# Performance work log

Measured on AMD Instinct MI355X. Metric: run time of the kernel, lower is better.

## Reference

```python
import jax, jax.numpy as jnp
import numpy as np

B = 8192; N = 50; NUM_NODES = 200000; NUM_EDGES = 1000000
FEAT = 64; EFEAT = 4; TD = 16; D = 64


def setup_inputs() -> dict:
    key = jax.random.key(0)
    ks = jax.random.split(key, 32)
    p = lambda i, shape: jax.random.normal(ks[i], shape, jnp.float32) * 0.05
    inp = {}
    nf = jax.random.normal(ks[0], (NUM_NODES, FEAT), jnp.float32)
    skills = jax.random.randint(ks[1], (NUM_NODES,), 0, 100).astype(jnp.float32)
    inp['node_raw_features'] = nf.at[:, 0].set(skills)  # col 0 = skill id
    inp['edge_raw_features'] = jax.random.normal(ks[2], (NUM_EDGES, EFEAT), jnp.float32)
    inp['src_node_ids'] = jax.random.randint(ks[3], (B,), 0, NUM_NODES)
    inp['dst_node_ids'] = jax.random.randint(ks[4], (B,), 0, NUM_NODES)
    inp['node_interact_times'] = jax.random.uniform(ks[5], (B,), jnp.float32, 0.0, 1e4)
    inp['src_neighbor_node_ids'] = jax.random.randint(ks[6], (B, N), 0, NUM_NODES)
    inp['src_neighbor_edge_ids'] = jax.random.randint(ks[7], (B, N), 0, NUM_EDGES)
    inp['src_neighbor_times'] = jax.random.uniform(ks[8], (B, N), jnp.float32, 0.0, 1e4)
    inp['dst_neighbor_node_ids'] = jax.random.randint(ks[9], (B, N), 0, NUM_NODES)
    inp['dst_neighbor_edge_ids'] = jax.random.randint(ks[10], (B, N), 0, NUM_EDGES)
    inp['dst_neighbor_times'] = jax.random.uniform(ks[11], (B, N), jnp.float32, 0.0, 1e4)
    # projection layers
    inp['W_feat'] = p(12, (FEAT, D)); inp['b_feat'] = p(13, (D,))
    inp['W_edge'] = p(14, (1, D));    inp['b_edge'] = p(15, (D,))
    inp['W_time'] = p(16, (TD, D));   inp['b_time'] = p(17, (D,))
    inp['W_struct'] = p(18, (1, D));  inp['b_struct'] = p(19, (D,))
    inp['W_out'] = p(20, (D, D));     inp['b_out'] = p(21, (D,))
    # time encoder (cos(w*dt + b), trainable Linear(1, TD) as in TGN TimeEncoder)
    inp['time_w'] = p(22, (TD,)); inp['time_b'] = p(23, (TD,))
    # src / dst GRUs (PyTorch layout: W_ih [3H,E], W_hh [3H,H])
    inp['src_W_ih'] = p(24, (3 * D, D)); inp['src_W_hh'] = p(25, (3 * D, D))
    inp['src_b_ih'] = p(26, (3 * D,));   inp['src_b_hh'] = p(27, (3 * D,))
    inp['dst_W_ih'] = p(28, (3 * D, D)); inp['dst_W_hh'] = p(29, (3 * D, D))
    inp['dst_b_ih'] = p(30, (3 * D,));   inp['dst_b_hh'] = p(31, (3 * D,))
    return inp


def _lin(x, W, b):
    return x @ W + b


def _gru_last_hidden(x, W_ih, W_hh, b_ih, b_hh):
    # x: [B, T, E] -> final hidden state [B, H] (PyTorch GRU equations)
    Bb, _, _ = x.shape
    H = W_hh.shape[1]

    def step(h, xt):
        gi = xt @ W_ih.T + b_ih            # [B, 3H]
        gh = h @ W_hh.T + b_hh             # [B, 3H]
        ir, iz, inn = jnp.split(gi, 3, axis=-1)
        hr, hz, hn = jnp.split(gh, 3, axis=-1)
        r = jax.nn.sigmoid(ir + hr)
        z = jax.nn.sigmoid(iz + hz)
        n = jnp.tanh(inn + r * hn)
        h_new = (1.0 - z) * n + z * h
        return h_new, None

    h0 = jnp.zeros((Bb, H), x.dtype)
    hT, _ = jax.lax.scan(step, h0, jnp.swapaxes(x, 0, 1))
    return hT


def reference(node_raw_features, edge_raw_features, src_node_ids, dst_node_ids,
              node_interact_times, src_neighbor_node_ids, src_neighbor_edge_ids,
              src_neighbor_times, dst_neighbor_node_ids, dst_neighbor_edge_ids,
              dst_neighbor_times, W_feat, b_feat, W_edge, b_edge, W_time, b_time,
              W_struct, b_struct, W_out, b_out, time_w, time_b,
              src_W_ih, src_W_hh, src_b_ih, src_b_hh,
              dst_W_ih, dst_W_hh, dst_b_ih, dst_b_hh):
    t = node_interact_times
    # append the query interaction itself (edge id 0) -> [B, N+1]
    src_nids = jnp.concatenate([src_neighbor_node_ids, src_node_ids[:, None]], 1)
    src_eids = jnp.concatenate([src_neighbor_edge_ids, jnp.zeros_like(src_node_ids)[:, None]], 1)
    src_ts = jnp.concatenate([src_neighbor_times, t[:, None]], 1)
    dst_nids = jnp.concatenate([dst_neighbor_node_ids, dst_node_ids[:, None]], 1)
    dst_eids = jnp.concatenate([dst_neighbor_edge_ids, jnp.zeros_like(dst_node_ids)[:, None]], 1)
    dst_ts = jnp.concatenate([dst_neighbor_times, t[:, None]], 1)

    # co-occurrence features [B, N, 1]
    co_src = (src_neighbor_node_ids == dst_node_ids[:, None]).astype(jnp.float32)[..., None]
    co_dst = (dst_neighbor_node_ids == src_node_ids[:, None]).astype(jnp.float32)[..., None]
    # skill match features [B, N, 1]
    src_skill = node_raw_features[src_nids][:, :-1, 0].astype(jnp.int32)
    dst_skill = node_raw_features[dst_nids][:, -1, 0].astype(jnp.int32)[:, None]
    skill_f = (src_skill == dst_skill).astype(jnp.float32)[..., None]

    src_struct = _lin(co_src, W_struct, b_struct)
    dst_struct = _lin(co_dst, W_struct, b_struct)
    skill_struct = _lin(skill_f, W_struct, b_struct)

    def get_feats(nids, eids, ts):
        node_f = _lin(node_raw_features[nids], W_feat, b_feat)        # [B,N+1,D]
        delta = t[:, None] - ts                                       # dual-decay ablation: delta times
        tenc = jnp.cos(delta[..., None] * time_w + time_b)            # [B,N+1,TD]
        time_f = _lin(tenc, W_time, b_time)                           # [B,N+1,D]
        edge_f = _lin(edge_raw_features[eids][..., :1], W_edge, b_edge)
        return node_f, edge_f, time_f

    sn, se, st = get_feats(src_nids, src_eids, src_ts)
    dn, de, dt = get_feats(dst_nids, dst_eids, dst_ts)
    src_feats = sn + se + st
    dst_feats = dn + de + dt

    src_emb = _gru_last_hidden(src_feats[:, :-1] + skill_struct + src_struct,
                               src_W_ih, src_W_hh, src_b_ih, src_b_hh) + (se + st)[:, -1]
    dst_emb = _gru_last_hidden((de + dt)[:, :-1] + dst_struct,
                               dst_W_ih, dst_W_hh, dst_b_ih, dst_b_hh) + dst_feats[:, -1]

    return _lin(src_emb, W_out, b_out), _lin(dst_emb, W_out, b_out)
```

## Files before the change

### kernel.cpp

```cpp
#include <hip/hip_runtime.h>
#include <stdint.h>

#define BB 8192
#define NN 50

typedef _Float16 half8 __attribute__((ext_vector_type(8)));
typedef float floatx4 __attribute__((ext_vector_type(4)));

union FragU { uint4 u; half8 h; };
static __device__ __forceinline__ half8 u2h(uint4 u) { FragU f; f.u = u; return f.h; }

static __device__ __forceinline__ uint32_t pk2u(float a, float b) {
    auto p = __builtin_amdgcn_cvt_pkrtz(a, b);
    uint32_t u; __builtin_memcpy(&u, &p, 4); return u;
}

#define MFMA(A, B, C) __builtin_amdgcn_mfma_f32_16x16x32_f16((A), (B), (C), 0, 0, 0)

static __device__ __forceinline__ float fsig(float x)   { return 1.0f / (1.0f + __expf(-x)); }
static __device__ __forceinline__ float ftanhf(float x) { return 1.0f - 2.0f / (__expf(2.0f * x) + 1.0f); }

__global__ __launch_bounds__(256, 1)
void dygkt3(const float* __restrict__ nodef, const float* __restrict__ edgef,
            const int* __restrict__ src_ids, const int* __restrict__ dst_ids,
            const float* __restrict__ times,
            const int* __restrict__ s_nids, const int* __restrict__ s_eids,
            const float* __restrict__ s_ts,
            const int* __restrict__ d_nids, const int* __restrict__ d_eids,
            const float* __restrict__ d_ts,
            const float* __restrict__ W_feat, const float* __restrict__ b_feat,
            const float* __restrict__ W_edge, const float* __restrict__ b_edge,
            const float* __restrict__ W_time, const float* __restrict__ b_time,
            const float* __restrict__ W_str,  const float* __restrict__ b_str,
            const float* __restrict__ W_out,  const float* __restrict__ b_out,
            const float* __restrict__ time_w, const float* __restrict__ time_b,
            const float* __restrict__ sWih, const float* __restrict__ sWhh,
            const float* __restrict__ sbih, const float* __restrict__ sbhh,
            const float* __restrict__ dWih, const float* __restrict__ dWhh,
            const float* __restrict__ dbih, const float* __restrict__ dbhh,
            float* __restrict__ out)
{
    __shared__ uint4 wfA[8][64];
    __shared__ uint4 woA[8][64];
    __shared__ __align__(16) _Float16 xbuf[4][16 * 72];
    __shared__ __align__(16) _Float16 hbuf[4][16 * 72];

    const int tid = threadIdx.x, wave = tid >> 6, lane = tid & 63;
    const int g = lane >> 4, i16 = lane & 15;
    const bool is_src = blockIdx.x < 128;
    const int ib0 = (int)(blockIdx.x & 127) * 64 + wave * 16;
    const int b = ib0 + i16;

    for (int q = tid; q < 512; q += 256) {
        int l = q & 63, tt = q >> 6;
        int kh = tt >> 2, mt = tt & 3, gg = l >> 4, ii = l & 15;
        float v[8], w[8];
        #pragma unroll
        for (int j = 0; j < 8; ++j) {
            int k = 32 * kh + 8 * gg + j, m = 16 * mt + ii;
            v[j] = W_feat[k * 64 + m];
            w[j] = W_out[k * 64 + m];
        }
        wfA[tt][l] = make_uint4(pk2u(v[0],v[1]), pk2u(v[2],v[3]), pk2u(v[4],v[5]), pk2u(v[6],v[7]));
        woA[tt][l] = make_uint4(pk2u(w[0],w[1]), pk2u(w[2],w[3]), pk2u(w[4],w[5]), pk2u(w[6],w[7]));
    }
    for (int q = tid; q < 4 * 16 * 72 / 2; q += 256) ((uint32_t*)hbuf)[q] = 0;
    __syncthreads();

    const float* WI = is_src ? sWih : dWih;
    const float* WH = is_src ? sWhh : dWhh;
    uint4 wih[12][2], whh[12][2];
    #pragma unroll
    for (int mt = 0; mt < 12; ++mt)
        #pragma unroll
        for (int kh = 0; kh < 2; ++kh) {
            const float* p = WI + (size_t)(16 * mt + i16) * 64 + 32 * kh + 8 * g;
            float4 a = *(const float4*)p, c = *(const float4*)(p + 4);
            wih[mt][kh] = make_uint4(pk2u(a.x,a.y), pk2u(a.z,a.w), pk2u(c.x,c.y), pk2u(c.z,c.w));
            const float* q = WH + (size_t)(16 * mt + i16) * 64 + 32 * kh + 8 * g;
            float4 e = *(const float4*)q, f = *(const float4*)(q + 4);
            whh[mt][kh] = make_uint4(pk2u(e.x,e.y), pk2u(e.z,e.w), pk2u(f.x,f.y), pk2u(f.z,f.w));
        }

    uint4 wtA[4];
    #pragma unroll
    for (int mt = 0; mt < 4; ++mt) {
        float v[8];
        #pragma unroll
        for (int j = 0; j < 8; ++j) {
            int k = 8 * g + j, dim = 16 * mt + i16;
            float x = 0.0f;
            if (k < 16)       x = W_time[k * 64 + dim];
            else if (k == 16) x = W_edge[dim];
            else if (k == 17) x = W_str[dim];
            else if (k == 18) x = b_edge[dim] + b_time[dim];
            else if (k == 19) x = is_src ? (b_feat[dim] + 2.0f * b_str[dim]) : b_str[dim];
            else if (k == 20) x = b_feat[dim];
            v[j] = x;
        }
        wtA[mt] = make_uint4(pk2u(v[0],v[1]), pk2u(v[2],v[3]), pk2u(v[4],v[5]), pk2u(v[6],v[7]));
    }

    const float* BI = is_src ? sbih : dbih;
    const float* BH = is_src ? sbhh : dbhh;
    floatx4 brz[8], bin[4], bhn[4];
    #pragma unroll
    for (int mt = 0; mt < 8; ++mt) {
        floatx4 v;
        #pragma unroll
        for (int r = 0; r < 4; ++r) v[r] = BI[16 * mt + 4 * g + r] + BH[16 * mt + 4 * g + r];
        brz[mt] = v;
    }
    #pragma unroll
    for (int mt = 0; mt < 4; ++mt) {
        floatx4 vi, vh;
        #pragma unroll
        for (int r = 0; r < 4; ++r) {
            vi[r] = BI[128 + 16 * mt + 4 * g + r];
            vh[r] = BH[128 + 16 * mt + 4 * g + r];
        }
        bin[mt] = vi; bhn[mt] = vh;
    }

    const int* pn = (is_src ? s_nids : d_nids) + (size_t)b * NN;
    const int* pe = (is_src ? s_eids : d_eids) + (size_t)b * NN;
    const float* pt = (is_src ? s_ts : d_ts) + (size_t)b * NN;
    const float tqL = times[b];
    const int didL = dst_ids[b];
    const int oid = is_src ? didL : src_ids[b];
    const float dskill = is_src ? nodef[(size_t)didL * 64] : 0.0f;
    float twc[8], tbc[8];
    #pragma unroll
    for (int j = 0; j < 8; ++j) {
        int k = 8 * (g & 1) + j;
        twc[j] = time_w[k]; tbc[j] = time_b[k];
    }

    int nidC = pn[0], eidC = pe[0];
    float tsC = pt[0];
    float e0C = edgef[4 * (size_t)eidC];
    float4 nfa = {0,0,0,0}, nfb = {0,0,0,0}, nfc = {0,0,0,0}, nfd = {0,0,0,0};
    if (is_src) {
        const float* rp = nodef + (size_t)nidC * 64 + 8 * g;
        nfa = *(const float4*)rp;        nfb = *(const float4*)(rp + 4);
        nfc = *(const float4*)(rp + 32); nfd = *(const float4*)(rp + 36);
    }

    floatx4 hM[4] = {{0,0,0,0},{0,0,0,0},{0,0,0,0},{0,0,0,0}};
    const floatx4 z4 = {0,0,0,0};
    _Float16* xb = xbuf[wave];
    _Float16* hb = hbuf[wave];

    for (int t = 0; t < NN; ++t) {
        int nidN = 0, eidN = 0; float tsN = 0.0f;
        if (t + 1 < NN) { nidN = pn[t + 1]; eidN = pe[t + 1]; tsN = pt[t + 1]; }

        float nsk = __shfl(nfa.x, i16);
        float sf = ((nidC == oid) ? 1.0f : 0.0f) +
                   ((is_src && nsk == dskill) ? 1.0f : 0.0f);
        float delta = tqL - tsC;
        uint4 tb4;
        if (g < 2) {
            float cv[8];
            #pragma unroll
            for (int j = 0; j < 8; ++j) cv[j] = __cosf(delta * twc[j] + tbc[j]);
            tb4 = make_uint4(pk2u(cv[0],cv[1]), pk2u(cv[2],cv[3]), pk2u(cv[4],cv[5]), pk2u(cv[6],cv[7]));
        } else if (g == 2) {
            tb4 = make_uint4(pk2u(e0C, sf), pk2u(1.0f, 1.0f), 0u, 0u);
        } else {
            tb4 = make_uint4(0u, 0u, 0u, 0u);
        }
        half8 tB = u2h(tb4);

        floatx4 xacc[4];
        if (is_src) {
            uint4 nf0 = make_uint4(pk2u(nfa.x,nfa.y), pk2u(nfa.z,nfa.w), pk2u(nfb.x,nfb.y), pk2u(nfb.z,nfb.w));
            uint4 nf1 = make_uint4(pk2u(nfc.x,nfc.y), pk2u(nfc.z,nfc.w), pk2u(nfd.x,nfd.y), pk2u(nfd.z,nfd.w));
            half8 nB0 = u2h(nf0), nB1 = u2h(nf1);
            #pragma unroll
            for (int mt = 0; mt < 4; ++mt) {
                floatx4 a = MFMA(u2h(wfA[mt][lane]), nB0, z4);
                a = MFMA(u2h(wfA[4 + mt][lane]), nB1, a);
                xacc[mt] = MFMA(u2h(wtA[mt]), tB, a);
            }
        } else {
            #pragma unroll
            for (int mt = 0; mt < 4; ++mt) xacc[mt] = MFMA(u2h(wtA[mt]), tB, z4);
        }

        #pragma unroll
        for (int mt = 0; mt < 4; ++mt)
            *(uint2*)&xb[i16 * 72 + mt * 16 + 4 * g] =
                make_uint2(pk2u(xacc[mt][0], xacc[mt][1]), pk2u(xacc[mt][2], xacc[mt][3]));
        half8 xB0 = u2h(*(const uint4*)&xb[i16 * 72 + 8 * g]);
        half8 xB1 = u2h(*(const uint4*)&xb[i16 * 72 + 32 + 8 * g]);

        float e0N = 0.0f; float4 na = {0,0,0,0}, nb = {0,0,0,0}, nc = {0,0,0,0}, nd = {0,0,0,0};
        if (t + 1 < NN) {
            e0N = edgef[4 * (size_t)eidN];
            if (is_src) {
                const float* rp = nodef + (size_t)nidN * 64 + 8 * g;
                na = *(const float4*)rp;        nb = *(const float4*)(rp + 4);
                nc = *(const float4*)(rp + 32); nd = *(const float4*)(rp + 36);
            }
        }

        half8 hB0 = u2h(*(const uint4*)&hb[i16 * 72 + 8 * g]);
        half8 hB1 = u2h(*(const uint4*)&hb[i16 * 72 + 32 + 8 * g]);

        floatx4 rg[4], zg[4], ia[4], ha[4];
        #pragma unroll
        for (int mt = 0; mt < 4; ++mt) {
            floatx4 a = MFMA(u2h(wih[mt][0]), xB0, brz[mt]);
            a = MFMA(u2h(wih[mt][1]), xB1, a);
            a = MFMA(u2h(whh[mt][0]), hB0, a);
            rg[mt] = MFMA(u2h(whh[mt][1]), hB1, a);
        }
        #pragma unroll
        for (int mt = 0; mt < 4; ++mt) {
            floatx4 a = MFMA(u2h(wih[4 + mt][0]), xB0, brz[4 + mt]);
            a = MFMA(u2h(wih[4 + mt][1]), xB1, a);
            a = MFMA(u2h(whh[4 + mt][0]), hB0, a);
            zg[mt] = MFMA(u2h(whh[4 + mt][1]), hB1, a);
        }
        #pragma unroll
        for (int mt = 0; mt < 4; ++mt) {
            floatx4 a = MFMA(u2h(wih[8 + mt][0]), xB0, bin[mt]);
            ia[mt] = MFMA(u2h(wih[8 + mt][1]), xB1, a);
            floatx4 c = MFMA(u2h(whh[8 + mt][0]), hB0, bhn[mt]);
            ha[mt] = MFMA(u2h(whh[8 + mt][1]), hB1, c);
        }

        #pragma unroll
        for (int mt = 0; mt < 4; ++mt)
            #pragma unroll
            for (int r = 0; r < 4; ++r) {
                float rr = fsig(rg[mt][r]);
                float zz = fsig(zg[mt][r]);
                float nn = ftanhf(ia[mt][r] + rr * ha[mt][r]);
                hM[mt][r] = nn + zz * (hM[mt][r] - nn);
            }

        #pragma unroll
        for (int mt = 0; mt < 4; ++mt)
            *(uint2*)&hb[i16 * 72 + mt * 16 + 4 * g] =
                make_uint2(pk2u(hM[mt][0], hM[mt][1]), pk2u(hM[mt][2], hM[mt][3]));

        nidC = nidN; eidC = eidN; tsC = tsN; e0C = e0N;
        nfa = na; nfb = nb; nfc = nc; nfd = nd;
    }

    float e00 = edgef[0];
    uint4 tt4;
    if (g < 2) {
        float cv[8];
        #pragma unroll
        for (int j = 0; j < 8; ++j) cv[j] = __cosf(tbc[j]);
        tt4 = make_uint4(pk2u(cv[0],cv[1]), pk2u(cv[2],cv[3]), pk2u(cv[4],cv[5]), pk2u(cv[6],cv[7]));
    } else if (g == 2) {
        tt4 = make_uint4(pk2u(e00, 0.0f), pk2u(1.0f, 0.0f), pk2u(is_src ? 0.0f : 1.0f, 0.0f), 0u);
    } else {
        tt4 = make_uint4(0u, 0u, 0u, 0u);
    }
    half8 tT = u2h(tt4);

    floatx4 tacc[4];
    #pragma unroll
    for (int mt = 0; mt < 4; ++mt) tacc[mt] = MFMA(u2h(wtA[mt]), tT, z4);
    if (!is_src) {
        const float* rp = nodef + (size_t)didL * 64 + 8 * g;
        float4 da = *(const float4*)rp,        db = *(const float4*)(rp + 4);
        float4 dc = *(const float4*)(rp + 32), dd = *(const float4*)(rp + 36);
        uint4 d0 = make_uint4(pk2u(da.x,da.y), pk2u(da.z,da.w), pk2u(db.x,db.y), pk2u(db.z,db.w));
        uint4 d1 = make_uint4(pk2u(dc.x,dc.y), pk2u(dc.z,dc.w), pk2u(dd.x,dd.y), pk2u(dd.z,dd.w));
        #pragma unroll
        for (int mt = 0; mt < 4; ++mt) {
            tacc[mt] = MFMA(u2h(wfA[mt][lane]), u2h(d0), tacc[mt]);
            tacc[mt] = MFMA(u2h(wfA[4 + mt][lane]), u2h(d1), tacc[mt]);
        }
    }

    #pragma unroll
    for (int mt = 0; mt < 4; ++mt) {
        floatx4 e = hM[mt] + tacc[mt];
        *(uint2*)&xb[i16 * 72 + mt * 16 + 4 * g] =
            make_uint2(pk2u(e[0], e[1]), pk2u(e[2], e[3]));
    }
    half8 eB0 = u2h(*(const uint4*)&xb[i16 * 72 + 8 * g]);
    half8 eB1 = u2h(*(const uint4*)&xb[i16 * 72 + 32 + 8 * g]);

    const size_t obase = (is_src ? 0 : (size_t)BB * 64) + (size_t)(ib0 + i16) * 64;
    #pragma unroll
    for (int mt = 0; mt < 4; ++mt) {
        floatx4 bo;
        #pragma unroll
        for (int r = 0; r < 4; ++r) bo[r] = b_out[16 * mt + 4 * g + r];
        floatx4 o = MFMA(u2h(woA[mt][lane]), eB0, bo);
        o = MFMA(u2h(woA[4 + mt][lane]), eB1, o);
        #pragma unroll
        for (int r = 0; r < 4; ++r)
            out[obase + 16 * mt + 4 * g + r] = o[r];
    }
}

extern "C" void kernel_launch(void* const* d_in, const int* in_sizes, int n_in,
                              void* d_out, int out_size, void* d_ws, size_t ws_size,
                              hipStream_t stream) {
    (void)in_sizes; (void)n_in; (void)d_ws; (void)ws_size; (void)out_size;
    const float* nodef  = (const float*)d_in[0];
    const float* edgef  = (const float*)d_in[1];
    const int*   srcid  = (const int*)  d_in[2];
    const int*   dstid  = (const int*)  d_in[3];
    const float* times  = (const float*)d_in[4];
    const int*   s_nids = (const int*)  d_in[5];
    const int*   s_eids = (const int*)  d_in[6];
    const float* s_ts   = (const float*)d_in[7];
    const int*   d_nids = (const int*)  d_in[8];
    const int*   d_eids = (const int*)  d_in[9];
    const float* d_ts   = (const float*)d_in[10];
    const float* W_feat = (const float*)d_in[11];
    const float* b_feat = (const float*)d_in[12];
    const float* W_edge = (const float*)d_in[13];
    const float* b_edge = (const float*)d_in[14];
    const float* W_time = (const float*)d_in[15];
    const float* b_time = (const float*)d_in[16];
    const float* W_str  = (const float*)d_in[17];
    const float* b_str  = (const float*)d_in[18];
    const float* W_out  = (const float*)d_in[19];
    const float* b_out  = (const float*)d_in[20];
    const float* time_w = (const float*)d_in[21];
    const float* time_b = (const float*)d_in[22];
    const float* sWih   = (const float*)d_in[23];
    const float* sWhh   = (const float*)d_in[24];
    const float* sbih   = (const float*)d_in[25];
    const float* sbhh   = (const float*)d_in[26];
    const float* dWih   = (const float*)d_in[27];
    const float* dWhh   = (const float*)d_in[28];
    const float* dbih   = (const float*)d_in[29];
    const float* dbhh   = (const float*)d_in[30];

    dim3 grid(256), block(256);
    dygkt3<<<grid, block, 0, stream>>>(
        nodef, edgef, srcid, dstid, times,
        s_nids, s_eids, s_ts, d_nids, d_eids, d_ts,
        W_feat, b_feat, W_edge, b_edge, W_time, b_time,
        W_str, b_str, W_out, b_out, time_w, time_b,
        sWih, sWhh, sbih, sbhh, dWih, dWhh, dbih, dbhh,
        (float*)d_out);
}
```

Baseline: 297.4 us.

## Fold input projections into GRU input weights and process two timesteps per iteration

Precomputes per block the products of the GRU input weights with W_feat and with the time/edge/struct/bias projections, stored in shared memory. Gate input preactivations then come directly from raw node features and time encodings, with no intermediate x vector. The loop handles two timesteps per iteration, computing both steps' input-gate contributions first and prefetching two steps ahead, which shortens the serial recurrent chain. The cost is fp16 rounding of the fused weights and gate inputs, a setup phase of MFMAs, and more registers and shared memory.

```diff
diff --git a/kernel.cpp b/kernel.cpp
--- a/kernel.cpp
+++ b/kernel.cpp
@@ -5,23 +5,34 @@
 #define NN 50
 
 typedef _Float16 half8 __attribute__((ext_vector_type(8)));
+typedef _Float16 half4v __attribute__((ext_vector_type(4)));
 typedef float floatx4 __attribute__((ext_vector_type(4)));
 
 union FragU { uint4 u; half8 h; };
 static __device__ __forceinline__ half8 u2h(uint4 u) { FragU f; f.u = u; return f.h; }
-
+union F2U { uint2 u; half4v h; };
+static __device__ __forceinline__ floatx4 up4(uint2 u) {
+    F2U f; f.u = u; floatx4 r;
+    r[0] = (float)f.h[0]; r[1] = (float)f.h[1]; r[2] = (float)f.h[2]; r[3] = (float)f.h[3];
+    return r;
+}
 static __device__ __forceinline__ uint32_t pk2u(float a, float b) {
     auto p = __builtin_amdgcn_cvt_pkrtz(a, b);
     uint32_t u; __builtin_memcpy(&u, &p, 4); return u;
 }
-
+static __device__ __forceinline__ uint2 pkx4(floatx4 v) {
+    return make_uint2(pk2u(v[0], v[1]), pk2u(v[2], v[3]));
+}
+static __device__ __forceinline__ uint4 pkf8(const float* p) {
+    float4 a = *(const float4*)p, b = *(const float4*)(p + 4);
+    return make_uint4(pk2u(a.x, a.y), pk2u(a.z, a.w), pk2u(b.x, b.y), pk2u(b.z, b.w));
+}
 #define MFMA(A, B, C) __builtin_amdgcn_mfma_f32_16x16x32_f16((A), (B), (C), 0, 0, 0)
-
 static __device__ __forceinline__ float fsig(float x)   { return 1.0f / (1.0f + __expf(-x)); }
 static __device__ __forceinline__ float ftanhf(float x) { return 1.0f - 2.0f / (__expf(2.0f * x) + 1.0f); }
 
 __global__ __launch_bounds__(256, 1)
-void dygkt3(const float* __restrict__ nodef, const float* __restrict__ edgef,
+void dygkt4(const float* __restrict__ nodef, const float* __restrict__ edgef,
             const int* __restrict__ src_ids, const int* __restrict__ dst_ids,
             const float* __restrict__ times,
             const int* __restrict__ s_nids, const int* __restrict__ s_eids,
@@ -40,88 +51,154 @@
             const float* __restrict__ dbih, const float* __restrict__ dbhh,
             float* __restrict__ out)
 {
-    __shared__ uint4 wfA[8][64];
-    __shared__ uint4 woA[8][64];
-    __shared__ __align__(16) _Float16 xbuf[4][16 * 72];
-    __shared__ __align__(16) _Float16 hbuf[4][16 * 72];
+    __shared__ _Float16 Gsh[192 * 72];
+    __shared__ _Float16 Bsh[192 * 40];
+    __shared__ uint4    woA[8][64];
+    __shared__ uint4    wtT[4][64];
+    __shared__ _Float16 hbuf[4 * 16 * 72];
 
     const int tid = threadIdx.x, wave = tid >> 6, lane = tid & 63;
     const int g = lane >> 4, i16 = lane & 15;
     const bool is_src = blockIdx.x < 128;
     const int ib0 = (int)(blockIdx.x & 127) * 64 + wave * 16;
     const int b = ib0 + i16;
+    const floatx4 z4 = {0, 0, 0, 0};
+
+    const float* WI = is_src ? sWih : dWih;
+    const float* WH = is_src ? sWhh : dWhh;
+    const float* BI = is_src ? sbih : dbih;
+    const float* BH = is_src ? sbhh : dbhh;
 
     for (int q = tid; q < 512; q += 256) {
         int l = q & 63, tt = q >> 6;
         int kh = tt >> 2, mt = tt & 3, gg = l >> 4, ii = l & 15;
-        float v[8], w[8];
+        float w[8];
+        #pragma unroll
+        for (int j = 0; j < 8; ++j)
+            w[j] = W_out[(32 * kh + 8 * gg + j) * 64 + 16 * mt + ii];
+        woA[tt][l] = make_uint4(pk2u(w[0],w[1]), pk2u(w[2],w[3]), pk2u(w[4],w[5]), pk2u(w[6],w[7]));
+    }
+    {
+        int l = tid & 63, mt = tid >> 6, gg = l >> 4, ii = l & 15;
+        float v[8];
         #pragma unroll
         for (int j = 0; j < 8; ++j) {
-            int k = 32 * kh + 8 * gg + j, m = 16 * mt + ii;
-            v[j] = W_feat[k * 64 + m];
-            w[j] = W_out[k * 64 + m];
-        }
-        wfA[tt][l] = make_uint4(pk2u(v[0],v[1]), pk2u(v[2],v[3]), pk2u(v[4],v[5]), pk2u(v[6],v[7]));
-        woA[tt][l] = make_uint4(pk2u(w[0],w[1]), pk2u(w[2],w[3]), pk2u(w[4],w[5]), pk2u(w[6],w[7]));
-    }
-    for (int q = tid; q < 4 * 16 * 72 / 2; q += 256) ((uint32_t*)hbuf)[q] = 0;
-    __syncthreads();
-
-    const float* WI = is_src ? sWih : dWih;
-    const float* WH = is_src ? sWhh : dWhh;
-    uint4 wih[12][2], whh[12][2];
-    #pragma unroll
-    for (int mt = 0; mt < 12; ++mt)
-        #pragma unroll
-        for (int kh = 0; kh < 2; ++kh) {
-            const float* p = WI + (size_t)(16 * mt + i16) * 64 + 32 * kh + 8 * g;
-            float4 a = *(const float4*)p, c = *(const float4*)(p + 4);
-            wih[mt][kh] = make_uint4(pk2u(a.x,a.y), pk2u(a.z,a.w), pk2u(c.x,c.y), pk2u(c.z,c.w));
-            const float* q = WH + (size_t)(16 * mt + i16) * 64 + 32 * kh + 8 * g;
-            float4 e = *(const float4*)q, f = *(const float4*)(q + 4);
-            whh[mt][kh] = make_uint4(pk2u(e.x,e.y), pk2u(e.z,e.w), pk2u(f.x,f.y), pk2u(f.z,f.w));
-        }
-
-    uint4 wtA[4];
-    #pragma unroll
-    for (int mt = 0; mt < 4; ++mt) {
-        float v[8];
-        #pragma unroll
-        for (int j = 0; j < 8; ++j) {
-            int k = 8 * g + j, dim = 16 * mt + i16;
+            int k = 8 * gg + j, dim = 16 * mt + ii;
             float x = 0.0f;
             if (k < 16)       x = W_time[k * 64 + dim];
             else if (k == 16) x = W_edge[dim];
             else if (k == 17) x = W_str[dim];
             else if (k == 18) x = b_edge[dim] + b_time[dim];
-            else if (k == 19) x = is_src ? (b_feat[dim] + 2.0f * b_str[dim]) : b_str[dim];
             else if (k == 20) x = b_feat[dim];
             v[j] = x;
         }
-        wtA[mt] = make_uint4(pk2u(v[0],v[1]), pk2u(v[2],v[3]), pk2u(v[4],v[5]), pk2u(v[6],v[7]));
-    }
-
-    const float* BI = is_src ? sbih : dbih;
-    const float* BH = is_src ? sbhh : dbhh;
-    floatx4 brz[8], bin[4], bhn[4];
-    #pragma unroll
-    for (int mt = 0; mt < 8; ++mt) {
+        wtT[mt][l] = make_uint4(pk2u(v[0],v[1]), pk2u(v[2],v[3]), pk2u(v[4],v[5]), pk2u(v[6],v[7]));
+    }
+    for (int q = tid; q < 2304; q += 256) ((uint32_t*)hbuf)[q] = 0;
+
+    uint4 whh[12][2];
+    #pragma unroll
+    for (int mt = 0; mt < 12; ++mt)
+        #pragma unroll
+        for (int kh = 0; kh < 2; ++kh)
+            whh[mt][kh] = pkf8(WH + (size_t)(16 * mt + i16) * 64 + 32 * kh + 8 * g);
+
+    if (is_src) {
+        for (int mt = wave; mt < 12; mt += 4) {
+            uint4 A0 = pkf8(WI + (size_t)(16 * mt + i16) * 64 + 8 * g);
+            uint4 A1 = pkf8(WI + (size_t)(16 * mt + i16) * 64 + 32 + 8 * g);
+            #pragma unroll
+            for (int nt = 0; nt < 4; ++nt) {
+                uint4 B0 = pkf8(W_feat + (size_t)(16 * nt + i16) * 64 + 8 * g);
+                uint4 B1 = pkf8(W_feat + (size_t)(16 * nt + i16) * 64 + 32 + 8 * g);
+                floatx4 D = MFMA(u2h(A1), u2h(B1), MFMA(u2h(A0), u2h(B0), z4));
+                #pragma unroll
+                for (int r = 0; r < 4; ++r)
+                    Gsh[(16 * mt + 4 * g + r) * 72 + 16 * nt + i16] = (_Float16)D[r];
+            }
+            #pragma unroll
+            for (int nt = 0; nt < 2; ++nt) {
+                uint4 bB[2];
+                #pragma unroll
+                for (int kh = 0; kh < 2; ++kh) {
+                    float v[8];
+                    #pragma unroll
+                    for (int jj = 0; jj < 8; ++jj) {
+                        int d = 32 * kh + 8 * g + jj;
+                        float x = 0.0f;
+                        if (nt == 0) x = W_time[i16 * 64 + d];
+                        else if (i16 == 0) x = W_edge[d];
+                        else if (i16 == 1) x = W_str[d];
+                        else if (i16 == 2) x = b_edge[d] + b_time[d] + b_feat[d] + 2.0f * b_str[d];
+                        v[jj] = x;
+                    }
+                    bB[kh] = make_uint4(pk2u(v[0],v[1]), pk2u(v[2],v[3]), pk2u(v[4],v[5]), pk2u(v[6],v[7]));
+                }
+                floatx4 D = MFMA(u2h(A1), u2h(bB[1]), MFMA(u2h(A0), u2h(bB[0]), z4));
+                if (nt == 1 && i16 == 2) {
+                    #pragma unroll
+                    for (int r = 0; r < 4; ++r)
+                        D[r] += BI[16 * mt + 4 * g + r] + (mt < 8 ? BH[16 * mt + 4 * g + r] : 0.0f);
+                }
+                #pragma unroll
+                for (int r = 0; r < 4; ++r)
+                    Bsh[(16 * mt + 4 * g + r) * 40 + 16 * nt + i16] = (_Float16)D[r];
+            }
+        }
+    } else {
+        for (int p = tid; p < 4096; p += 256) {
+            int m = p & 63, j = p >> 6;
+            Gsh[m * 72 + j] = (_Float16)W_feat[j * 64 + m];
+        }
+        for (int mt = wave; mt < 12; mt += 4) {
+            uint4 A0 = pkf8(WI + (size_t)(16 * mt + i16) * 64 + 8 * g);
+            uint4 A1 = pkf8(WI + (size_t)(16 * mt + i16) * 64 + 32 + 8 * g);
+            #pragma unroll
+            for (int nt = 0; nt < 2; ++nt) {
+                uint4 bB[2];
+                #pragma unroll
+                for (int kh = 0; kh < 2; ++kh) {
+                    float v[8];
+                    #pragma unroll
+                    for (int jj = 0; jj < 8; ++jj) {
+                        int d = 32 * kh + 8 * g + jj;
+                        float x = 0.0f;
+                        if (nt == 0) x = W_time[i16 * 64 + d];
+                        else if (i16 == 0) x = W_edge[d];
+                        else if (i16 == 1) x = W_str[d];
+                        else if (i16 == 2) x = b_edge[d] + b_time[d] + b_str[d];
+                        v[jj] = x;
+                    }
+                    bB[kh] = make_uint4(pk2u(v[0],v[1]), pk2u(v[2],v[3]), pk2u(v[4],v[5]), pk2u(v[6],v[7]));
+                }
+                floatx4 D = MFMA(u2h(A1), u2h(bB[1]), MFMA(u2h(A0), u2h(bB[0]), z4));
+                if (nt == 1 && i16 == 2) {
+                    #pragma unroll
+                    for (int r = 0; r < 4; ++r)
+                        D[r] += BI[16 * mt + 4 * g + r] + (mt < 8 ? BH[16 * mt + 4 * g + r] : 0.0f);
+                }
+                #pragma unroll
+                for (int r = 0; r < 4; ++r)
+                    Bsh[(16 * mt + 4 * g + r) * 40 + 16 * nt + i16] = (_Float16)D[r];
+            }
+        }
+    }
+    __syncthreads();
+
+    floatx4 bhn[4];
+    #pragma unroll
+    for (int mt = 0; mt < 4; ++mt) {
         floatx4 v;
         #pragma unroll
-        for (int r = 0; r < 4; ++r) v[r] = BI[16 * mt + 4 * g + r] + BH[16 * mt + 4 * g + r];
-        brz[mt] = v;
-    }
-    #pragma unroll
-    for (int mt = 0; mt < 4; ++mt) {
-        floatx4 vi, vh;
-        #pragma unroll
-        for (int r = 0; r < 4; ++r) {
-            vi[r] = BI[128 + 16 * mt + 4 * g + r];
-            vh[r] = BH[128 + 16 * mt + 4 * g + r];
-        }
-        bin[mt] = vi; bhn[mt] = vh;
-    }
-
+        for (int r = 0; r < 4; ++r) v[r] = BH[128 + 16 * mt + 4 * g + r];
+        bhn[mt] = v;
+    }
+    float twc[8], tbc[8];
+    #pragma unroll
+    for (int j = 0; j < 8; ++j) {
+        twc[j] = time_w[8 * (g & 1) + j];
+        tbc[j] = time_b[8 * (g & 1) + j];
+    }
     const int* pn = (is_src ? s_nids : d_nids) + (size_t)b * NN;
     const int* pe = (is_src ? s_eids : d_eids) + (size_t)b * NN;
     const float* pt = (is_src ? s_ts : d_ts) + (size_t)b * NN;
@@ -129,125 +206,126 @@
     const int didL = dst_ids[b];
     const int oid = is_src ? didL : src_ids[b];
     const float dskill = is_src ? nodef[(size_t)didL * 64] : 0.0f;
-    float twc[8], tbc[8];
-    #pragma unroll
-    for (int j = 0; j < 8; ++j) {
-        int k = 8 * (g & 1) + j;
-        twc[j] = time_w[k]; tbc[j] = time_b[k];
-    }
-
-    int nidC = pn[0], eidC = pe[0];
-    float tsC = pt[0];
-    float e0C = edgef[4 * (size_t)eidC];
-    float4 nfa = {0,0,0,0}, nfb = {0,0,0,0}, nfc = {0,0,0,0}, nfd = {0,0,0,0};
-    if (is_src) {
-        const float* rp = nodef + (size_t)nidC * 64 + 8 * g;
-        nfa = *(const float4*)rp;        nfb = *(const float4*)(rp + 4);
-        nfc = *(const float4*)(rp + 32); nfd = *(const float4*)(rp + 36);
+
+    _Float16* hb = hbuf + wave * (16 * 72);
+
+    int nidS[2]; float tsS[2], e0S[2], nskS[2];
+    uint4 nf0S[2], nf1S[2];
+    #pragma unroll
+    for (int s = 0; s < 2; ++s) {
+        nidS[s] = pn[s]; tsS[s] = pt[s];
+        e0S[s] = edgef[4 * (size_t)pe[s]];
+        nskS[s] = 0.0f; nf0S[s] = make_uint4(0,0,0,0); nf1S[s] = make_uint4(0,0,0,0);
+        if (is_src) {
+            const float* rp = nodef + (size_t)nidS[s] * 64 + 8 * g;
+            float4 a = *(const float4*)rp,        c = *(const float4*)(rp + 4);
+            float4 d = *(const float4*)(rp + 32), e = *(const float4*)(rp + 36);
+            nskS[s] = __shfl(a.x, i16);
+            nf0S[s] = make_uint4(pk2u(a.x,a.y), pk2u(a.z,a.w), pk2u(c.x,c.y), pk2u(c.z,c.w));
+            nf1S[s] = make_uint4(pk2u(d.x,d.y), pk2u(d.z,d.w), pk2u(e.x,e.y), pk2u(e.z,e.w));
+        }
     }
 
     floatx4 hM[4] = {{0,0,0,0},{0,0,0,0},{0,0,0,0},{0,0,0,0}};
-    const floatx4 z4 = {0,0,0,0};
-    _Float16* xb = xbuf[wave];
-    _Float16* hb = hbuf[wave];
-
-    for (int t = 0; t < NN; ++t) {
-        int nidN = 0, eidN = 0; float tsN = 0.0f;
-        if (t + 1 < NN) { nidN = pn[t + 1]; eidN = pe[t + 1]; tsN = pt[t + 1]; }
-
-        float nsk = __shfl(nfa.x, i16);
-        float sf = ((nidC == oid) ? 1.0f : 0.0f) +
-                   ((is_src && nsk == dskill) ? 1.0f : 0.0f);
-        float delta = tqL - tsC;
-        uint4 tb4;
-        if (g < 2) {
-            float cv[8];
-            #pragma unroll
-            for (int j = 0; j < 8; ++j) cv[j] = __cosf(delta * twc[j] + tbc[j]);
-            tb4 = make_uint4(pk2u(cv[0],cv[1]), pk2u(cv[2],cv[3]), pk2u(cv[4],cv[5]), pk2u(cv[6],cv[7]));
-        } else if (g == 2) {
-            tb4 = make_uint4(pk2u(e0C, sf), pk2u(1.0f, 1.0f), 0u, 0u);
-        } else {
-            tb4 = make_uint4(0u, 0u, 0u, 0u);
-        }
-        half8 tB = u2h(tb4);
-
-        floatx4 xacc[4];
-        if (is_src) {
-            uint4 nf0 = make_uint4(pk2u(nfa.x,nfa.y), pk2u(nfa.z,nfa.w), pk2u(nfb.x,nfb.y), pk2u(nfb.z,nfb.w));
-            uint4 nf1 = make_uint4(pk2u(nfc.x,nfc.y), pk2u(nfc.z,nfc.w), pk2u(nfd.x,nfd.y), pk2u(nfd.z,nfd.w));
-            half8 nB0 = u2h(nf0), nB1 = u2h(nf1);
+
+    for (int tb = 0; tb < 25; ++tb) {
+        int nidN[2] = {0, 0}; float tsN[2] = {0, 0}, e0N[2] = {0, 0};
+        float4 ra[2], rb[2], rc[2], rd[2];
+        const bool pf = (tb < 24);
+        if (pf) {
+            #pragma unroll
+            for (int s = 0; s < 2; ++s) {
+                int t2 = 2 * tb + 2 + s;
+                nidN[s] = pn[t2]; tsN[s] = pt[t2];
+                e0N[s] = edgef[4 * (size_t)pe[t2]];
+                if (is_src) {
+                    const float* rp = nodef + (size_t)nidN[s] * 64 + 8 * g;
+                    ra[s] = *(const float4*)rp;        rb[s] = *(const float4*)(rp + 4);
+                    rc[s] = *(const float4*)(rp + 32); rd[s] = *(const float4*)(rp + 36);
+                }
+            }
+        }
+
+        uint4 tv[2];
+        #pragma unroll
+        for (int s = 0; s < 2; ++s) {
+            float sf = ((nidS[s] == oid) ? 1.0f : 0.0f) +
+                       ((is_src && nskS[s] == dskill) ? 1.0f : 0.0f);
+            float delta = tqL - tsS[s];
+            if (g < 2) {
+                float cv[8];
+                #pragma unroll
+                for (int j = 0; j < 8; ++j) cv[j] = __cosf(delta * twc[j] + tbc[j]);
+                tv[s] = make_uint4(pk2u(cv[0],cv[1]), pk2u(cv[2],cv[3]), pk2u(cv[4],cv[5]), pk2u(cv[6],cv[7]));
+            } else if (g == 2) {
+                tv[s] = make_uint4(pk2u(e0S[s], sf), pk2u(1.0f, 0.0f), 0u, 0u);
+            } else {
+                tv[s] = make_uint4(0u, 0u, 0u, 0u);
+            }
+        }
+        uint2 giP[2][12];
+        #pragma unroll
+        for (int mt = 0; mt < 12; ++mt) {
+            uint4 BA = *(const uint4*)&Bsh[(16 * mt + i16) * 40 + 8 * g];
+            floatx4 a0 = MFMA(u2h(BA), u2h(tv[0]), z4);
+            floatx4 a1 = MFMA(u2h(BA), u2h(tv[1]), z4);
+            if (is_src) {
+                uint4 G0 = *(const uint4*)&Gsh[(16 * mt + i16) * 72 + 8 * g];
+                uint4 G1 = *(const uint4*)&Gsh[(16 * mt + i16) * 72 + 32 + 8 * g];
+                a0 = MFMA(u2h(G0), u2h(nf0S[0]), a0);
+                a0 = MFMA(u2h(G1), u2h(nf1S[0]), a0);
+                a1 = MFMA(u2h(G0), u2h(nf0S[1]), a1);
+                a1 = MFMA(u2h(G1), u2h(nf1S[1]), a1);
+            }
+            giP[0][mt] = pkx4(a0);
+            giP[1][mt] = pkx4(a1);
+        }
+
+        if (pf) {
+            #pragma unroll
+            for (int s = 0; s < 2; ++s) {
+                nidS[s] = nidN[s]; tsS[s] = tsN[s]; e0S[s] = e0N[s];
+                if (is_src) {
+                    nskS[s] = __shfl(ra[s].x, i16);
+                    nf0S[s] = make_uint4(pk2u(ra[s].x,ra[s].y), pk2u(ra[s].z,ra[s].w),
+                                         pk2u(rb[s].x,rb[s].y), pk2u(rb[s].z,rb[s].w));
+                    nf1S[s] = make_uint4(pk2u(rc[s].x,rc[s].y), pk2u(rc[s].z,rc[s].w),
+                                         pk2u(rd[s].x,rd[s].y), pk2u(rd[s].z,rd[s].w));
+                }
+            }
+        }
+
+        #pragma unroll
+        for (int s = 0; s < 2; ++s) {
+            half8 hB0 = u2h(*(const uint4*)&hb[i16 * 72 + 8 * g]);
+            half8 hB1 = u2h(*(const uint4*)&hb[i16 * 72 + 32 + 8 * g]);
+            floatx4 ga[12];
+            #pragma unroll
+            for (int mt = 0; mt < 8; ++mt) {
+                floatx4 c = up4(giP[s][mt]);
+                c = MFMA(u2h(whh[mt][0]), hB0, c);
+                ga[mt] = MFMA(u2h(whh[mt][1]), hB1, c);
+            }
+            #pragma unroll
+            for (int mt = 8; mt < 12; ++mt) {
+                floatx4 c = MFMA(u2h(whh[mt][0]), hB0, bhn[mt - 8]);
+                ga[mt] = MFMA(u2h(whh[mt][1]), hB1, c);
+            }
             #pragma unroll
             for (int mt = 0; mt < 4; ++mt) {
-                floatx4 a = MFMA(u2h(wfA[mt][lane]), nB0, z4);
-                a = MFMA(u2h(wfA[4 + mt][lane]), nB1, a);
-                xacc[mt] = MFMA(u2h(wtA[mt]), tB, a);
-            }
-        } else {
-            #pragma unroll
-            for (int mt = 0; mt < 4; ++mt) xacc[mt] = MFMA(u2h(wtA[mt]), tB, z4);
-        }
-
-        #pragma unroll
-        for (int mt = 0; mt < 4; ++mt)
-            *(uint2*)&xb[i16 * 72 + mt * 16 + 4 * g] =
-                make_uint2(pk2u(xacc[mt][0], xacc[mt][1]), pk2u(xacc[mt][2], xacc[mt][3]));
-        half8 xB0 = u2h(*(const uint4*)&xb[i16 * 72 + 8 * g]);
-        half8 xB1 = u2h(*(const uint4*)&xb[i16 * 72 + 32 + 8 * g]);
-
-        float e0N = 0.0f; float4 na = {0,0,0,0}, nb = {0,0,0,0}, nc = {0,0,0,0}, nd = {0,0,0,0};
-        if (t + 1 < NN) {
-            e0N = edgef[4 * (size_t)eidN];
-            if (is_src) {
-                const float* rp = nodef + (size_t)nidN * 64 + 8 * g;
-                na = *(const float4*)rp;        nb = *(const float4*)(rp + 4);
-                nc = *(const float4*)(rp + 32); nd = *(const float4*)(rp + 36);
-            }
-        }
-
-        half8 hB0 = u2h(*(const uint4*)&hb[i16 * 72 + 8 * g]);
-        half8 hB1 = u2h(*(const uint4*)&hb[i16 * 72 + 32 + 8 * g]);
-
-        floatx4 rg[4], zg[4], ia[4], ha[4];
-        #pragma unroll
-        for (int mt = 0; mt < 4; ++mt) {
-            floatx4 a = MFMA(u2h(wih[mt][0]), xB0, brz[mt]);
-            a = MFMA(u2h(wih[mt][1]), xB1, a);
-            a = MFMA(u2h(whh[mt][0]), hB0, a);
-            rg[mt] = MFMA(u2h(whh[mt][1]), hB1, a);
-        }
-        #pragma unroll
-        for (int mt = 0; mt < 4; ++mt) {
-            floatx4 a = MFMA(u2h(wih[4 + mt][0]), xB0, brz[4 + mt]);
-            a = MFMA(u2h(wih[4 + mt][1]), xB1, a);
-            a = MFMA(u2h(whh[4 + mt][0]), hB0, a);
-            zg[mt] = MFMA(u2h(whh[4 + mt][1]), hB1, a);
-        }
-        #pragma unroll
-        for (int mt = 0; mt < 4; ++mt) {
-            floatx4 a = MFMA(u2h(wih[8 + mt][0]), xB0, bin[mt]);
-            ia[mt] = MFMA(u2h(wih[8 + mt][1]), xB1, a);
-            floatx4 c = MFMA(u2h(whh[8 + mt][0]), hB0, bhn[mt]);
-            ha[mt] = MFMA(u2h(whh[8 + mt][1]), hB1, c);
-        }
-
-        #pragma unroll
-        for (int mt = 0; mt < 4; ++mt)
-            #pragma unroll
-            for (int r = 0; r < 4; ++r) {
-                float rr = fsig(rg[mt][r]);
-                float zz = fsig(zg[mt][r]);
-                float nn = ftanhf(ia[mt][r] + rr * ha[mt][r]);
-                hM[mt][r] = nn + zz * (hM[mt][r] - nn);
-            }
-
-        #pragma unroll
-        for (int mt = 0; mt < 4; ++mt)
-            *(uint2*)&hb[i16 * 72 + mt * 16 + 4 * g] =
-                make_uint2(pk2u(hM[mt][0], hM[mt][1]), pk2u(hM[mt][2], hM[mt][3]));
-
-        nidC = nidN; eidC = eidN; tsC = tsN; e0C = e0N;
-        nfa = na; nfb = nb; nfc = nc; nfd = nd;
+                floatx4 gin = up4(giP[s][8 + mt]);
+                #pragma unroll
+                for (int r = 0; r < 4; ++r) {
+                    float rr = fsig(ga[mt][r]);
+                    float zz = fsig(ga[4 + mt][r]);
+                    float nn = ftanhf(gin[r] + rr * ga[8 + mt][r]);
+                    hM[mt][r] = nn + zz * (hM[mt][r] - nn);
+                }
+            }
+            #pragma unroll
+            for (int mt = 0; mt < 4; ++mt)
+                *(uint2*)&hb[i16 * 72 + 16 * mt + 4 * g] = pkx4(hM[mt]);
+        }
     }
 
     float e00 = edgef[0];
@@ -266,28 +344,29 @@
 
     floatx4 tacc[4];
     #pragma unroll
-    for (int mt = 0; mt < 4; ++mt) tacc[mt] = MFMA(u2h(wtA[mt]), tT, z4);
+    for (int mt = 0; mt < 4; ++mt) tacc[mt] = MFMA(u2h(wtT[mt][lane]), tT, z4);
     if (!is_src) {
         const float* rp = nodef + (size_t)didL * 64 + 8 * g;
-        float4 da = *(const float4*)rp,        db = *(const float4*)(rp + 4);
-        float4 dc = *(const float4*)(rp + 32), dd = *(const float4*)(rp + 36);
-        uint4 d0 = make_uint4(pk2u(da.x,da.y), pk2u(da.z,da.w), pk2u(db.x,db.y), pk2u(db.z,db.w));
-        uint4 d1 = make_uint4(pk2u(dc.x,dc.y), pk2u(dc.z,dc.w), pk2u(dd.x,dd.y), pk2u(dd.z,dd.w));
+        float4 a = *(const float4*)rp,        c = *(const float4*)(rp + 4);
+        float4 d = *(const float4*)(rp + 32), e = *(const float4*)(rp + 36);
+        uint4 d0 = make_uint4(pk2u(a.x,a.y), pk2u(a.z,a.w), pk2u(c.x,c.y), pk2u(c.z,c.w));
+        uint4 d1 = make_uint4(pk2u(d.x,d.y), pk2u(d.z,d.w), pk2u(e.x,e.y), pk2u(e.z,e.w));
         #pragma unroll
         for (int mt = 0; mt < 4; ++mt) {
-            tacc[mt] = MFMA(u2h(wfA[mt][lane]), u2h(d0), tacc[mt]);
-            tacc[mt] = MFMA(u2h(wfA[4 + mt][lane]), u2h(d1), tacc[mt]);
+            uint4 G0 = *(const uint4*)&Gsh[(16 * mt + i16) * 72 + 8 * g];
+            uint4 G1 = *(const uint4*)&Gsh[(16 * mt + i16) * 72 + 32 + 8 * g];
+            tacc[mt] = MFMA(u2h(G0), u2h(d0), tacc[mt]);
+            tacc[mt] = MFMA(u2h(G1), u2h(d1), tacc[mt]);
         }
     }
 
     #pragma unroll
     for (int mt = 0; mt < 4; ++mt) {
-        floatx4 e = hM[mt] + tacc[mt];
-        *(uint2*)&xb[i16 * 72 + mt * 16 + 4 * g] =
-            make_uint2(pk2u(e[0], e[1]), pk2u(e[2], e[3]));
-    }
-    half8 eB0 = u2h(*(const uint4*)&xb[i16 * 72 + 8 * g]);
-    half8 eB1 = u2h(*(const uint4*)&xb[i16 * 72 + 32 + 8 * g]);
+        floatx4 e4 = hM[mt] + tacc[mt];
+        *(uint2*)&hb[i16 * 72 + 16 * mt + 4 * g] = pkx4(e4);
+    }
+    half8 eB0 = u2h(*(const uint4*)&hb[i16 * 72 + 8 * g]);
+    half8 eB1 = u2h(*(const uint4*)&hb[i16 * 72 + 32 + 8 * g]);
 
     const size_t obase = (is_src ? 0 : (size_t)BB * 64) + (size_t)(ib0 + i16) * 64;
     #pragma unroll
@@ -340,7 +419,7 @@
     const float* dbhh   = (const float*)d_in[30];
 
     dim3 grid(256), block(256);
-    dygkt3<<<grid, block, 0, stream>>>(
+    dygkt4<<<grid, block, 0, stream>>>(
         nodef, edgef, srcid, dstid, times,
         s_nids, s_eids, s_ts, d_nids, d_eids, d_ts,
         W_feat, b_feat, W_edge, b_edge, W_time, b_time,
```

After: 350.9 us. 1.18x slower.
